# Optimization experiments

Hardware: AMD Instinct MI355X
Metric: run time of the kernel (lower is better)

## Reference

```python
import jax, jax.numpy as jnp
import numpy as np

B, D, U = 256, 2048, 2048  # batch, input_dim, units
EPS = 1e-8


def setup_inputs() -> dict:
    key = jax.random.key(0)
    ks = jax.random.split(key, 20)
    sd = 1.0 / np.sqrt(D)
    su = 1.0 / np.sqrt(U)
    inp = {
        'x': jax.random.normal(ks[0], (B, D), jnp.float32),
        'h_prev': jax.random.normal(ks[1], (B, U), jnp.float32),
        'c_prev': jax.random.normal(ks[2], (B, U), jnp.float32),
        'n_prev': jax.random.uniform(ks[3], (B, U), jnp.float32),
        'm_prev': jax.random.normal(ks[4], (B, U), jnp.float32),
        # input-to-gate weights (Dense with bias), keras layout [in, out]
        'Wz': jax.random.normal(ks[5], (D, U), jnp.float32) * sd,
        'Wi': jax.random.normal(ks[6], (D, U), jnp.float32) * sd,
        'Wf': jax.random.normal(ks[7], (D, U), jnp.float32) * sd,
        'Wo': jax.random.normal(ks[8], (D, U), jnp.float32) * sd,
        'bz': jnp.zeros((U,), jnp.float32),
        'bi': jnp.zeros((U,), jnp.float32),
        'bf': jnp.zeros((U,), jnp.float32),
        'bo': jnp.zeros((U,), jnp.float32),
        # recurrent weights (Dense without bias)
        'Uz': jax.random.normal(ks[9], (U, U), jnp.float32) * su,
        'Ui': jax.random.normal(ks[10], (U, U), jnp.float32) * su,
        'Uf': jax.random.normal(ks[11], (U, U), jnp.float32) * su,
        'Uo': jax.random.normal(ks[12], (U, U), jnp.float32) * su,
    }
    return inp


def reference(x, h_prev, c_prev, n_prev, m_prev,
              Wz, Wi, Wf, Wo, bz, bi, bf, bo, Uz, Ui, Uf, Uo):
    # fuse the 8 small GEMMs into 2 wide GEMMs (same math, gates split after)
    W = jnp.concatenate([Wz, Wi, Wf, Wo], axis=1)      # [D, 4U]
    Uc = jnp.concatenate([Uz, Ui, Uf, Uo], axis=1)     # [U, 4U]
    b = jnp.concatenate([bz, bi, bf, bo], axis=0)      # [4U]
    pre = x @ W + h_prev @ Uc + b                      # [B, 4U]
    z_tilde, i_tilde, f_tilde, o_tilde = jnp.split(pre, 4, axis=1)

    # exponential-gate stabilization (forget_gate_type='exponential')
    m_t = jnp.maximum(i_tilde + m_prev, i_tilde)
    i_t = jnp.exp(i_tilde - m_t)
    f_t = jnp.exp(f_tilde + m_prev - m_t)

    o_t = jax.nn.sigmoid(o_tilde)
    z_t = jnp.tanh(z_tilde)

    c_t = f_t * c_prev + i_t * z_t
    n_t = f_t * n_prev + i_t
    h_t = o_t * (c_t / (n_t + EPS))
    return jnp.stack([h_t, c_t, n_t, m_t], axis=0)  # [4, B, U]
```

## Files before the change

### kernel.cpp

```cpp
#include <hip/hip_runtime.h>
#include <cstdint>
#include <cstddef>

#define B_   256
#define D_   2048
#define U_   2048
#define NTOT 8192
#define BN   32
#define BK   64
#define KC   2048
#define ITERS (KC / BK)

typedef _Float16 half8 __attribute__((ext_vector_type(8)));
typedef float floatx16 __attribute__((ext_vector_type(16)));

__global__ __launch_bounds__(256) void prep_kernel(
    const float* __restrict__ x, const float* __restrict__ h,
    _Float16* __restrict__ Ahi)
{
    int gid   = blockIdx.x * 256 + threadIdx.x;
    int chunk = gid >> 8;
    int row   = gid & 255;
    int col0  = chunk * 8;
    const float* src = (col0 < D_) ? (x + row * D_ + col0)
                                   : (h + row * U_ + (col0 - D_));
    float4 v0 = *(const float4*)(src);
    float4 v1 = *(const float4*)(src + 4);
    float v[8] = {v0.x, v0.y, v0.z, v0.w, v1.x, v1.y, v1.z, v1.w};
    half8 hi;
#pragma unroll
    for (int i = 0; i < 8; ++i) hi[i] = (_Float16)v[i];
    *(half8*)(Ahi + (chunk * 256 + row) * 8) = hi;
}

__global__ __launch_bounds__(256, 2) void gemm_kernel(
    const _Float16* __restrict__ Ahi,
    const float* __restrict__ Wz, const float* __restrict__ Wi,
    const float* __restrict__ Wf, const float* __restrict__ Wo,
    const float* __restrict__ Uz, const float* __restrict__ Ui,
    const float* __restrict__ Uf, const float* __restrict__ Uo,
    float* __restrict__ P)
{
    __shared__ __align__(16) _Float16 sA[2][8 * 256 * 8];
    __shared__ __align__(16) _Float16 sB[2][BK * BN];

    const int t    = threadIdx.x;
    const int w    = t >> 6;
    const int lane = t & 63;
    const int lg   = lane >> 5;
    const int lm   = lane & 31;

    const int nblk = blockIdx.x;
    const int ks   = blockIdx.y;
    const int n0   = nblk * BN;
    const int g    = n0 >> 11;
    const int c0   = n0 & (U_ - 1);

    const float* wsel[8] = {Wz, Wi, Wf, Wo, Uz, Ui, Uf, Uo};
    const float* Bm = wsel[ks * 4 + g];
    const int chunk0 = ks * 256;

    const _Float16* Ag = Ahi + (size_t)chunk0 * 2048
                             + (size_t)(w * 8) * 512 + (size_t)lane * 8;

    const int scol = t & 31;
    const int sk0  = (t >> 5) * 8;
    const float* Bg = Bm + (size_t)sk0 * U_ + c0 + scol;
    const int swb = scol * 128 + ((sk0 * 2) ^ ((scol & 7) << 4));
    const int bswz = (lm & 7) << 4;

    const int aoff = lg * 4096 + (w * 64 + lm) * 16;

    floatx16 acc0 = {}, acc1 = {};
    float rbA[8], rbB[8];

#define ISSUE_A(tt, buf)                                                      \
    {                                                                         \
        _Pragma("unroll")                                                     \
        for (int i = 0; i < 8; ++i)                                           \
            __builtin_amdgcn_global_load_lds(                                 \
                (const __attribute__((address_space(1))) void*)(              \
                    Ag + (size_t)(tt) * 16384 + i * 512),                     \
                (__attribute__((address_space(3))) void*)(                    \
                    (char*)&sA[buf][0] + (w * 8 + i) * 1024 + lane * 16),     \
                16, 0, 0);                                                    \
    }

#define ISSUE_B(tt, rb)                                                       \
    {                                                                         \
        _Pragma("unroll")                                                     \
        for (int j = 0; j < 8; ++j)                                           \
            rb[j] = Bg[((size_t)(tt) * 64 + j) * U_];                         \
    }

#define WRITE_B(rb, buf)                                                      \
    {                                                                         \
        half8 hv;                                                             \
        _Pragma("unroll")                                                     \
        for (int j = 0; j < 8; ++j) hv[j] = (_Float16)rb[j];                  \
        *(half8*)((char*)&sB[buf][0] + swb) = hv;                             \
    }

#define COMPUTE(cur)                                                          \
    {                                                                         \
        const char* bA = (const char*)&sA[cur][0];                            \
        const char* bB = (const char*)&sB[cur][0];                            \
        half8 af0[4], af1[4], bfr[4];                                         \
        _Pragma("unroll")                                                     \
        for (int kin = 0; kin < 4; ++kin) {                                   \
            af0[kin] = *(const half8*)(bA + aoff + kin * 8192);               \
            af1[kin] = *(const half8*)(bA + aoff + kin * 8192 + 512);         \
            bfr[kin] = *(const half8*)(bB + lm * 128 +                        \
                ((kin * 32 + lg * 16) ^ bswz));                               \
        }                                                                     \
        __builtin_amdgcn_s_setprio(1);                                        \
        _Pragma("unroll")                                                     \
        for (int kin = 0; kin < 4; ++kin) {                                   \
            acc0 = __builtin_amdgcn_mfma_f32_32x32x16_f16(af0[kin], bfr[kin], acc0, 0, 0, 0); \
            acc1 = __builtin_amdgcn_mfma_f32_32x32x16_f16(af1[kin], bfr[kin], acc1, 0, 0, 0); \
        }                                                                     \
        __builtin_amdgcn_s_setprio(0);                                        \
    }

    ISSUE_B(0, rbA);
    ISSUE_A(0, 0);
    ISSUE_B(1, rbB);
    WRITE_B(rbA, 0);
    asm volatile("s_waitcnt vmcnt(8) lgkmcnt(0)" ::: "memory");
    __builtin_amdgcn_s_barrier();

    for (int tt = 0; tt < ITERS - 2; tt += 2) {
        ISSUE_A(tt + 1, 1);
        ISSUE_B(tt + 2, rbA);
        COMPUTE(0);
        WRITE_B(rbB, 1);
        asm volatile("s_waitcnt vmcnt(8) lgkmcnt(0)" ::: "memory");
        __builtin_amdgcn_s_barrier();

        ISSUE_A(tt + 2, 0);
        ISSUE_B(tt + 3, rbB);
        COMPUTE(1);
        WRITE_B(rbA, 0);
        asm volatile("s_waitcnt vmcnt(8) lgkmcnt(0)" ::: "memory");
        __builtin_amdgcn_s_barrier();
    }

    ISSUE_A(ITERS - 1, 1);
    COMPUTE(0);
    WRITE_B(rbB, 1);
    asm volatile("s_waitcnt vmcnt(0) lgkmcnt(0)" ::: "memory");
    __builtin_amdgcn_s_barrier();
    COMPUTE(1);

#undef ISSUE_A
#undef ISSUE_B
#undef WRITE_B
#undef COMPUTE

    float* Pks = P + (size_t)ks * ((size_t)B_ * NTOT);
#pragma unroll
    for (int r = 0; r < 16; ++r) {
        int m = w * 64 + 4 * lg + (r & 3) + 8 * (r >> 2);
        Pks[(size_t)m * NTOT + n0 + lm] = acc0[r];
    }
#pragma unroll
    for (int r = 0; r < 16; ++r) {
        int m = w * 64 + 32 + 4 * lg + (r & 3) + 8 * (r >> 2);
        Pks[(size_t)m * NTOT + n0 + lm] = acc1[r];
    }
}

__global__ __launch_bounds__(256) void gates_kernel(
    const float* __restrict__ P,
    const float* __restrict__ c_prev, const float* __restrict__ n_prev,
    const float* __restrict__ m_prev,
    const float* __restrict__ bz, const float* __restrict__ bi,
    const float* __restrict__ bf, const float* __restrict__ bo,
    float* __restrict__ out)
{
    const size_t PS = (size_t)B_ * NTOT;
    const int OS = B_ * U_;
    int gid = blockIdx.x * 256 + threadIdx.x;
    int m = gid >> 9;
    int u = (gid & 511) * 4;

    float pre[4][4];
#pragma unroll
    for (int gi = 0; gi < 4; ++gi) {
        const float* base = P + (size_t)m * NTOT + gi * U_ + u;
        float4 s0 = *(const float4*)(base);
        float4 s1 = *(const float4*)(base + PS);
        pre[gi][0] = s0.x + s1.x;
        pre[gi][1] = s0.y + s1.y;
        pre[gi][2] = s0.z + s1.z;
        pre[gi][3] = s0.w + s1.w;
    }
    float4 bzv = *(const float4*)(bz + u);
    float4 biv = *(const float4*)(bi + u);
    float4 bfv = *(const float4*)(bf + u);
    float4 bov = *(const float4*)(bo + u);
    float bza[4] = {bzv.x, bzv.y, bzv.z, bzv.w};
    float bia[4] = {biv.x, biv.y, biv.z, biv.w};
    float bfa[4] = {bfv.x, bfv.y, bfv.z, bfv.w};
    float boa[4] = {bov.x, bov.y, bov.z, bov.w};

    float4 cp4 = *(const float4*)(c_prev + m * U_ + u);
    float4 np4 = *(const float4*)(n_prev + m * U_ + u);
    float4 mp4 = *(const float4*)(m_prev + m * U_ + u);
    float cpa[4] = {cp4.x, cp4.y, cp4.z, cp4.w};
    float npa[4] = {np4.x, np4.y, np4.z, np4.w};
    float mpa[4] = {mp4.x, mp4.y, mp4.z, mp4.w};

    float hr[4], cr[4], nr[4], mr[4];
#pragma unroll
    for (int e = 0; e < 4; ++e) {
        float zt = pre[0][e] + bza[e];
        float it = pre[1][e] + bia[e];
        float ft = pre[2][e] + bfa[e];
        float ot = pre[3][e] + boa[e];
        float mp = mpa[e];
        float m_t = fmaxf(it + mp, it);
        float i_t = expf(it - m_t);
        float f_t = expf(ft + mp - m_t);
        float o_t = 1.0f / (1.0f + expf(-ot));
        float z_t = tanhf(zt);
        float c_t = f_t * cpa[e] + i_t * z_t;
        float n_t = f_t * npa[e] + i_t;
        float h_t = o_t * (c_t / (n_t + 1e-8f));
        hr[e] = h_t; cr[e] = c_t; nr[e] = n_t; mr[e] = m_t;
    }
    float4 hv = {hr[0], hr[1], hr[2], hr[3]};
    float4 cv = {cr[0], cr[1], cr[2], cr[3]};
    float4 nv = {nr[0], nr[1], nr[2], nr[3]};
    float4 mv = {mr[0], mr[1], mr[2], mr[3]};
    *(float4*)(out + 0 * OS + m * U_ + u) = hv;
    *(float4*)(out + 1 * OS + m * U_ + u) = cv;
    *(float4*)(out + 2 * OS + m * U_ + u) = nv;
    *(float4*)(out + 3 * OS + m * U_ + u) = mv;
}

extern "C" void kernel_launch(void* const* d_in, const int* in_sizes, int n_in,
                              void* d_out, int out_size, void* d_ws, size_t ws_size,
                              hipStream_t stream)
{
    const float* x  = (const float*)d_in[0];
    const float* h  = (const float*)d_in[1];
    const float* cp = (const float*)d_in[2];
    const float* np = (const float*)d_in[3];
    const float* mp = (const float*)d_in[4];
    const float* Wz = (const float*)d_in[5];
    const float* Wi = (const float*)d_in[6];
    const float* Wf = (const float*)d_in[7];
    const float* Wo = (const float*)d_in[8];
    const float* bz = (const float*)d_in[9];
    const float* bi = (const float*)d_in[10];
    const float* bf = (const float*)d_in[11];
    const float* bo = (const float*)d_in[12];
    const float* Uz = (const float*)d_in[13];
    const float* Ui = (const float*)d_in[14];
    const float* Uf = (const float*)d_in[15];
    const float* Uo = (const float*)d_in[16];

    float* P = (float*)d_ws;
    _Float16* Ahi = (_Float16*)((char*)d_ws + (size_t)2 * B_ * NTOT * sizeof(float));

    prep_kernel<<<512, 256, 0, stream>>>(x, h, Ahi);
    gemm_kernel<<<dim3(256, 2), 256, 0, stream>>>(Ahi,
        Wz, Wi, Wf, Wo, Uz, Ui, Uf, Uo, P);
    gates_kernel<<<512, 256, 0, stream>>>(P, cp, np, mp, bz, bi, bf, bo,
        (float*)d_out);
}
```

Measured before the change: 213.1 us.

## Give each wave its own A LDS slice and split vmcnt waits around compute

The A tile in shared memory is re-laid out so each wave loads and reads only its own contiguous slice, without the previous cross-wave interleave. The B-tile swizzle changes from an XOR pattern to a rotation. The single combined vmcnt/lgkmcnt wait before each barrier is split into separate vmcnt waits placed just before COMPUTE and WRITE_B, plus an lgkmcnt wait. The goal is to stop stalling on loads that the next step does not need yet, so global fetches overlap more with MFMA work. The new wait counts depend on exact issue order, and a miscount could read stale data; the new layout could also bring different LDS bank conflicts.

New measurement: 216.3 us. Within noise of the previous version (+1.5%).

```diff
diff --git a/kernel.cpp b/kernel.cpp
--- a/kernel.cpp
+++ b/kernel.cpp
@@ -41,7 +41,7 @@
     const float* __restrict__ Uf, const float* __restrict__ Uo,
     float* __restrict__ P)
 {
-    __shared__ __align__(16) _Float16 sA[2][8 * 256 * 8];
+    __shared__ __align__(16) _Float16 sA[2][4 * 8 * 64 * 8];
     __shared__ __align__(16) _Float16 sB[2][BK * BN];
 
     const int t    = threadIdx.x;
@@ -61,15 +61,12 @@
     const int chunk0 = ks * 256;
 
     const _Float16* Ag = Ahi + (size_t)chunk0 * 2048
-                             + (size_t)(w * 8) * 512 + (size_t)lane * 8;
+                             + (size_t)w * 512 + (size_t)lane * 8;
 
     const int scol = t & 31;
     const int sk0  = (t >> 5) * 8;
     const float* Bg = Bm + (size_t)sk0 * U_ + c0 + scol;
-    const int swb = scol * 128 + ((sk0 * 2) ^ ((scol & 7) << 4));
-    const int bswz = (lm & 7) << 4;
-
-    const int aoff = lg * 4096 + (w * 64 + lm) * 16;
+    const int swb = scol * 128 + ((sk0 * 2 + ((scol >> 2) << 4)) & 127);
 
     floatx16 acc0 = {}, acc1 = {};
     float rbA[8], rbB[8];
@@ -77,12 +74,12 @@
 #define ISSUE_A(tt, buf)                                                      \
     {                                                                         \
         _Pragma("unroll")                                                     \
-        for (int i = 0; i < 8; ++i)                                           \
+        for (int c = 0; c < 8; ++c)                                           \
             __builtin_amdgcn_global_load_lds(                                 \
                 (const __attribute__((address_space(1))) void*)(              \
-                    Ag + (size_t)(tt) * 16384 + i * 512),                     \
+                    Ag + (size_t)(tt) * 16384 + c * 2048),                    \
                 (__attribute__((address_space(3))) void*)(                    \
-                    (char*)&sA[buf][0] + (w * 8 + i) * 1024 + lane * 16),     \
+                    &sA[buf][w * 4096 + c * 512 + lane * 8]),                 \
                 16, 0, 0);                                                    \
     }
 
@@ -103,15 +100,15 @@
 
 #define COMPUTE(cur)                                                          \
     {                                                                         \
-        const char* bA = (const char*)&sA[cur][0];                            \
-        const char* bB = (const char*)&sB[cur][0];                            \
+        const _Float16* wA = &sA[cur][w * 4096];                              \
+        const char*     bB = (const char*)&sB[cur][0];                        \
         half8 af0[4], af1[4], bfr[4];                                         \
         _Pragma("unroll")                                                     \
         for (int kin = 0; kin < 4; ++kin) {                                   \
-            af0[kin] = *(const half8*)(bA + aoff + kin * 8192);               \
-            af1[kin] = *(const half8*)(bA + aoff + kin * 8192 + 512);         \
+            af0[kin] = *(const half8*)(wA + (kin * 2 + lg) * 512 + lm * 8);   \
+            af1[kin] = *(const half8*)(wA + (kin * 2 + lg) * 512 + lm * 8 + 256); \
             bfr[kin] = *(const half8*)(bB + lm * 128 +                        \
-                ((kin * 32 + lg * 16) ^ bswz));                               \
+                ((kin * 32 + lg * 16 + ((lm >> 2) << 4)) & 127));             \
         }                                                                     \
         __builtin_amdgcn_s_setprio(1);                                        \
         _Pragma("unroll")                                                     \
@@ -122,34 +119,42 @@
         __builtin_amdgcn_s_setprio(0);                                        \
     }
 
+    ISSUE_A(0, 0);
     ISSUE_B(0, rbA);
-    ISSUE_A(0, 0);
     ISSUE_B(1, rbB);
+    asm volatile("s_waitcnt vmcnt(8)" ::: "memory");
     WRITE_B(rbA, 0);
-    asm volatile("s_waitcnt vmcnt(8) lgkmcnt(0)" ::: "memory");
+    asm volatile("s_waitcnt lgkmcnt(0)" ::: "memory");
     __builtin_amdgcn_s_barrier();
 
     for (int tt = 0; tt < ITERS - 2; tt += 2) {
         ISSUE_A(tt + 1, 1);
         ISSUE_B(tt + 2, rbA);
+        asm volatile("s_waitcnt vmcnt(24)" ::: "memory");
         COMPUTE(0);
+        asm volatile("s_waitcnt vmcnt(16)" ::: "memory");
         WRITE_B(rbB, 1);
-        asm volatile("s_waitcnt vmcnt(8) lgkmcnt(0)" ::: "memory");
+        asm volatile("s_waitcnt lgkmcnt(0)" ::: "memory");
         __builtin_amdgcn_s_barrier();
 
         ISSUE_A(tt + 2, 0);
         ISSUE_B(tt + 3, rbB);
+        asm volatile("s_waitcnt vmcnt(24)" ::: "memory");
         COMPUTE(1);
+        asm volatile("s_waitcnt vmcnt(16)" ::: "memory");
         WRITE_B(rbA, 0);
-        asm volatile("s_waitcnt vmcnt(8) lgkmcnt(0)" ::: "memory");
+        asm volatile("s_waitcnt lgkmcnt(0)" ::: "memory");
         __builtin_amdgcn_s_barrier();
     }
 
     ISSUE_A(ITERS - 1, 1);
+    asm volatile("s_waitcnt vmcnt(16)" ::: "memory");
     COMPUTE(0);
+    asm volatile("s_waitcnt vmcnt(8)" ::: "memory");
     WRITE_B(rbB, 1);
-    asm volatile("s_waitcnt vmcnt(0) lgkmcnt(0)" ::: "memory");
+    asm volatile("s_waitcnt lgkmcnt(0)" ::: "memory");
     __builtin_amdgcn_s_barrier();
+    asm volatile("s_waitcnt vmcnt(0)" ::: "memory");
     COMPUTE(1);
 
 #undef ISSUE_A
```

## Retile GEMM to 128x128 blocks with 4-way split-K and fp16 partials

Applied to the files above, without the earlier changes.

Replaces the 256x32 full-batch tile (split-K 2) with 128x128 tiles over a 2x2 wave grid and split-K of 4. Each block now loads a quarter of the activation rows but four times as many weight columns, which cuts redundant A traffic through LDS. Partial sums are written as fp16 instead of fp32, halving workspace traffic, and the gates kernel sums four fp16 partials with 8 elements per thread. The cost is lower precision in the partial sums, more split-K reduction reads, and a block order that interleaves M tiles.

Result: faster. 206.2 us (-3.3%).

```diff
diff --git a/kernel.cpp b/kernel.cpp
--- a/kernel.cpp
+++ b/kernel.cpp
@@ -6,9 +6,11 @@
 #define D_   2048
 #define U_   2048
 #define NTOT 8192
-#define BN   32
+#define BM   128
+#define BN   128
 #define BK   64
-#define KC   2048
+#define KSP  4
+#define KC   1024
 #define ITERS (KC / BK)
 
 typedef _Float16 half8 __attribute__((ext_vector_type(8)));
@@ -33,91 +35,100 @@
     *(half8*)(Ahi + (chunk * 256 + row) * 8) = hi;
 }
 
-__global__ __launch_bounds__(256, 2) void gemm_kernel(
+__global__ __launch_bounds__(256) void gemm_kernel(
     const _Float16* __restrict__ Ahi,
     const float* __restrict__ Wz, const float* __restrict__ Wi,
     const float* __restrict__ Wf, const float* __restrict__ Wo,
     const float* __restrict__ Uz, const float* __restrict__ Ui,
     const float* __restrict__ Uf, const float* __restrict__ Uo,
-    float* __restrict__ P)
-{
-    __shared__ __align__(16) _Float16 sA[2][8 * 256 * 8];
-    __shared__ __align__(16) _Float16 sB[2][BK * BN];
+    _Float16* __restrict__ P)
+{
+    __shared__ __align__(16) _Float16 sA[2][8 * 128 * 8];
+    __shared__ __align__(16) _Float16 sB[2][8 * 128 * 8];
 
     const int t    = threadIdx.x;
     const int w    = t >> 6;
     const int lane = t & 63;
     const int lg   = lane >> 5;
     const int lm   = lane & 31;
-
-    const int nblk = blockIdx.x;
-    const int ks   = blockIdx.y;
-    const int n0   = nblk * BN;
-    const int g    = n0 >> 11;
-    const int c0   = n0 & (U_ - 1);
+    const int wm   = w >> 1;
+    const int wn   = w & 1;
+
+    const int bx = blockIdx.x;
+    const int mt = (bx >> 3) & 1;
+    const int nt = ((bx >> 4) << 3) | (bx & 7);
+    const int ks = blockIdx.y;
+
+    const int m0 = mt * BM;
+    const int n0 = nt * BN;
+    const int g  = n0 >> 11;
+    const int c0 = n0 & (U_ - 1);
 
     const float* wsel[8] = {Wz, Wi, Wf, Wo, Uz, Ui, Uf, Uo};
-    const float* Bm = wsel[ks * 4 + g];
-    const int chunk0 = ks * 256;
-
-    const _Float16* Ag = Ahi + (size_t)chunk0 * 2048
-                             + (size_t)(w * 8) * 512 + (size_t)lane * 8;
-
-    const int scol = t & 31;
-    const int sk0  = (t >> 5) * 8;
-    const float* Bg = Bm + (size_t)sk0 * U_ + c0 + scol;
-    const int swb = scol * 128 + ((sk0 * 2) ^ ((scol & 7) << 4));
-    const int bswz = (lm & 7) << 4;
-
-    const int aoff = lg * 4096 + (w * 64 + lm) * 16;
-
-    floatx16 acc0 = {}, acc1 = {};
-    float rbA[8], rbB[8];
+    const float* Bm = wsel[(ks >> 1) * 4 + g];
+    const int km = (ks & 1) * 1024;
+    const int chunkbase = ks * 128;
+
+    const int arow  = t & 127;
+    const int ahalf = t >> 7;
+
+    const int bcol  = t & 127;
+    const int sbase = (t >> 7) * 4;
+    const float* Bg = Bm + (size_t)km * U_ + c0 + bcol;
+
+    floatx16 acc00 = {}, acc01 = {}, acc10 = {}, acc11 = {};
+    float rbA[32], rbB[32];
 
 #define ISSUE_A(tt, buf)                                                      \
     {                                                                         \
         _Pragma("unroll")                                                     \
-        for (int i = 0; i < 8; ++i)                                           \
+        for (int i = 0; i < 4; ++i) {                                         \
+            int c = 2 * i + ahalf;                                            \
             __builtin_amdgcn_global_load_lds(                                 \
                 (const __attribute__((address_space(1))) void*)(              \
-                    Ag + (size_t)(tt) * 16384 + i * 512),                     \
+                    Ahi + (size_t)(chunkbase + (tt) * 8 + c) * 2048           \
+                        + (m0 + arow) * 8),                                   \
                 (__attribute__((address_space(3))) void*)(                    \
-                    (char*)&sA[buf][0] + (w * 8 + i) * 1024 + lane * 16),     \
+                    &sA[buf][i * 2048 + t * 8]),                              \
                 16, 0, 0);                                                    \
+        }                                                                     \
     }
 
 #define ISSUE_B(tt, rb)                                                       \
     {                                                                         \
         _Pragma("unroll")                                                     \
-        for (int j = 0; j < 8; ++j)                                           \
-            rb[j] = Bg[((size_t)(tt) * 64 + j) * U_];                         \
+        for (int sc = 0; sc < 4; ++sc)                                        \
+            _Pragma("unroll")                                                 \
+            for (int j = 0; j < 8; ++j)                                       \
+                rb[sc * 8 + j] =                                              \
+                    Bg[(size_t)((tt) * 64 + (sbase + sc) * 8 + j) * U_];      \
     }
 
 #define WRITE_B(rb, buf)                                                      \
     {                                                                         \
-        half8 hv;                                                             \
-        _Pragma("unroll")                                                     \
-        for (int j = 0; j < 8; ++j) hv[j] = (_Float16)rb[j];                  \
-        *(half8*)((char*)&sB[buf][0] + swb) = hv;                             \
+        _Pragma("unroll")                                                     \
+        for (int sc = 0; sc < 4; ++sc) {                                      \
+            half8 hv;                                                         \
+            _Pragma("unroll")                                                 \
+            for (int j = 0; j < 8; ++j) hv[j] = (_Float16)rb[sc * 8 + j];     \
+            *(half8*)(&sB[buf][(sbase + sc) * 1024 + bcol * 8]) = hv;         \
+        }                                                                     \
     }
 
 #define COMPUTE(cur)                                                          \
     {                                                                         \
-        const char* bA = (const char*)&sA[cur][0];                            \
-        const char* bB = (const char*)&sB[cur][0];                            \
-        half8 af0[4], af1[4], bfr[4];                                         \
+        __builtin_amdgcn_s_setprio(1);                                        \
         _Pragma("unroll")                                                     \
         for (int kin = 0; kin < 4; ++kin) {                                   \
-            af0[kin] = *(const half8*)(bA + aoff + kin * 8192);               \
-            af1[kin] = *(const half8*)(bA + aoff + kin * 8192 + 512);         \
-            bfr[kin] = *(const half8*)(bB + lm * 128 +                        \
-                ((kin * 32 + lg * 16) ^ bswz));                               \
-        }                                                                     \
-        __builtin_amdgcn_s_setprio(1);                                        \
-        _Pragma("unroll")                                                     \
-        for (int kin = 0; kin < 4; ++kin) {                                   \
-            acc0 = __builtin_amdgcn_mfma_f32_32x32x16_f16(af0[kin], bfr[kin], acc0, 0, 0, 0); \
-            acc1 = __builtin_amdgcn_mfma_f32_32x32x16_f16(af1[kin], bfr[kin], acc1, 0, 0, 0); \
+            int cs = kin * 2 + lg;                                            \
+            half8 a0 = *(const half8*)(&sA[cur][cs * 1024 + (wm * 64 + lm) * 8]);       \
+            half8 a1 = *(const half8*)(&sA[cur][cs * 1024 + (wm * 64 + 32 + lm) * 8]);  \
+            half8 b0 = *(const half8*)(&sB[cur][cs * 1024 + (wn * 64 + lm) * 8]);       \
+            half8 b1 = *(const half8*)(&sB[cur][cs * 1024 + (wn * 64 + 32 + lm) * 8]);  \
+            acc00 = __builtin_amdgcn_mfma_f32_32x32x16_f16(a0, b0, acc00, 0, 0, 0);     \
+            acc01 = __builtin_amdgcn_mfma_f32_32x32x16_f16(a0, b1, acc01, 0, 0, 0);     \
+            acc10 = __builtin_amdgcn_mfma_f32_32x32x16_f16(a1, b0, acc10, 0, 0, 0);     \
+            acc11 = __builtin_amdgcn_mfma_f32_32x32x16_f16(a1, b1, acc11, 0, 0, 0);     \
         }                                                                     \
         __builtin_amdgcn_s_setprio(0);                                        \
     }
@@ -125,28 +136,32 @@
     ISSUE_B(0, rbA);
     ISSUE_A(0, 0);
     ISSUE_B(1, rbB);
+    asm volatile("s_waitcnt vmcnt(36)" ::: "memory");
     WRITE_B(rbA, 0);
-    asm volatile("s_waitcnt vmcnt(8) lgkmcnt(0)" ::: "memory");
+    asm volatile("s_waitcnt vmcnt(32) lgkmcnt(0)" ::: "memory");
     __builtin_amdgcn_s_barrier();
 
     for (int tt = 0; tt < ITERS - 2; tt += 2) {
         ISSUE_A(tt + 1, 1);
         ISSUE_B(tt + 2, rbA);
         COMPUTE(0);
+        asm volatile("s_waitcnt vmcnt(36)" ::: "memory");
         WRITE_B(rbB, 1);
-        asm volatile("s_waitcnt vmcnt(8) lgkmcnt(0)" ::: "memory");
+        asm volatile("s_waitcnt vmcnt(32) lgkmcnt(0)" ::: "memory");
         __builtin_amdgcn_s_barrier();
 
         ISSUE_A(tt + 2, 0);
         ISSUE_B(tt + 3, rbB);
         COMPUTE(1);
+        asm volatile("s_waitcnt vmcnt(36)" ::: "memory");
         WRITE_B(rbA, 0);
-        asm volatile("s_waitcnt vmcnt(8) lgkmcnt(0)" ::: "memory");
+        asm volatile("s_waitcnt vmcnt(32) lgkmcnt(0)" ::: "memory");
         __builtin_amdgcn_s_barrier();
     }
 
     ISSUE_A(ITERS - 1, 1);
     COMPUTE(0);
+    asm volatile("s_waitcnt vmcnt(4)" ::: "memory");
     WRITE_B(rbB, 1);
     asm volatile("s_waitcnt vmcnt(0) lgkmcnt(0)" ::: "memory");
     __builtin_amdgcn_s_barrier();
@@ -157,21 +172,24 @@
 #undef WRITE_B
 #undef COMPUTE
 
-    float* Pks = P + (size_t)ks * ((size_t)B_ * NTOT);
-#pragma unroll
-    for (int r = 0; r < 16; ++r) {
-        int m = w * 64 + 4 * lg + (r & 3) + 8 * (r >> 2);
-        Pks[(size_t)m * NTOT + n0 + lm] = acc0[r];
-    }
-#pragma unroll
-    for (int r = 0; r < 16; ++r) {
-        int m = w * 64 + 32 + 4 * lg + (r & 3) + 8 * (r >> 2);
-        Pks[(size_t)m * NTOT + n0 + lm] = acc1[r];
-    }
+    _Float16* Pks = P + (size_t)ks * ((size_t)B_ * NTOT);
+    const floatx16* accs[4] = {&acc00, &acc01, &acc10, &acc11};
+#pragma unroll
+    for (int mi = 0; mi < 2; ++mi)
+#pragma unroll
+        for (int ni = 0; ni < 2; ++ni) {
+            const floatx16& a = *accs[mi * 2 + ni];
+            int colg = n0 + wn * 64 + ni * 32 + lm;
+#pragma unroll
+            for (int r = 0; r < 16; ++r) {
+                int m = m0 + wm * 64 + mi * 32 + 4 * lg + (r & 3) + 8 * (r >> 2);
+                Pks[(size_t)m * NTOT + colg] = (_Float16)a[r];
+            }
+        }
 }
 
 __global__ __launch_bounds__(256) void gates_kernel(
-    const float* __restrict__ P,
+    const _Float16* __restrict__ P,
     const float* __restrict__ c_prev, const float* __restrict__ n_prev,
     const float* __restrict__ m_prev,
     const float* __restrict__ bz, const float* __restrict__ bi,
@@ -181,39 +199,42 @@
     const size_t PS = (size_t)B_ * NTOT;
     const int OS = B_ * U_;
     int gid = blockIdx.x * 256 + threadIdx.x;
-    int m = gid >> 9;
-    int u = (gid & 511) * 4;
-
-    float pre[4][4];
+    int m = gid >> 8;
+    int u = (gid & 255) * 8;
+
+    float pre[4][8];
 #pragma unroll
     for (int gi = 0; gi < 4; ++gi) {
-        const float* base = P + (size_t)m * NTOT + gi * U_ + u;
-        float4 s0 = *(const float4*)(base);
-        float4 s1 = *(const float4*)(base + PS);
-        pre[gi][0] = s0.x + s1.x;
-        pre[gi][1] = s0.y + s1.y;
-        pre[gi][2] = s0.z + s1.z;
-        pre[gi][3] = s0.w + s1.w;
-    }
-    float4 bzv = *(const float4*)(bz + u);
-    float4 biv = *(const float4*)(bi + u);
-    float4 bfv = *(const float4*)(bf + u);
-    float4 bov = *(const float4*)(bo + u);
-    float bza[4] = {bzv.x, bzv.y, bzv.z, bzv.w};
-    float bia[4] = {biv.x, biv.y, biv.z, biv.w};
-    float bfa[4] = {bfv.x, bfv.y, bfv.z, bfv.w};
-    float boa[4] = {bov.x, bov.y, bov.z, bov.w};
-
-    float4 cp4 = *(const float4*)(c_prev + m * U_ + u);
-    float4 np4 = *(const float4*)(n_prev + m * U_ + u);
-    float4 mp4 = *(const float4*)(m_prev + m * U_ + u);
-    float cpa[4] = {cp4.x, cp4.y, cp4.z, cp4.w};
-    float npa[4] = {np4.x, np4.y, np4.z, np4.w};
-    float mpa[4] = {mp4.x, mp4.y, mp4.z, mp4.w};
-
-    float hr[4], cr[4], nr[4], mr[4];
-#pragma unroll
-    for (int e = 0; e < 4; ++e) {
+#pragma unroll
+        for (int e = 0; e < 8; ++e) pre[gi][e] = 0.0f;
+#pragma unroll
+        for (int ksp = 0; ksp < 4; ++ksp) {
+            half8 v = *(const half8*)(P + (size_t)ksp * PS
+                                        + (size_t)m * NTOT + gi * 2048 + u);
+#pragma unroll
+            for (int e = 0; e < 8; ++e) pre[gi][e] += (float)v[e];
+        }
+    }
+
+    float bza[8], bia[8], bfa[8], boa[8], cpa[8], npa[8], mpa[8];
+    *(float4*)(bza)     = *(const float4*)(bz + u);
+    *(float4*)(bza + 4) = *(const float4*)(bz + u + 4);
+    *(float4*)(bia)     = *(const float4*)(bi + u);
+    *(float4*)(bia + 4) = *(const float4*)(bi + u + 4);
+    *(float4*)(bfa)     = *(const float4*)(bf + u);
+    *(float4*)(bfa + 4) = *(const float4*)(bf + u + 4);
+    *(float4*)(boa)     = *(const float4*)(bo + u);
+    *(float4*)(boa + 4) = *(const float4*)(bo + u + 4);
+    *(float4*)(cpa)     = *(const float4*)(c_prev + m * U_ + u);
+    *(float4*)(cpa + 4) = *(const float4*)(c_prev + m * U_ + u + 4);
+    *(float4*)(npa)     = *(const float4*)(n_prev + m * U_ + u);
+    *(float4*)(npa + 4) = *(const float4*)(n_prev + m * U_ + u + 4);
+    *(float4*)(mpa)     = *(const float4*)(m_prev + m * U_ + u);
+    *(float4*)(mpa + 4) = *(const float4*)(m_prev + m * U_ + u + 4);
+
+    float hr[8], cr[8], nr[8], mr[8];
+#pragma unroll
+    for (int e = 0; e < 8; ++e) {
         float zt = pre[0][e] + bza[e];
         float it = pre[1][e] + bia[e];
         float ft = pre[2][e] + bfa[e];
@@ -229,14 +250,15 @@
         float h_t = o_t * (c_t / (n_t + 1e-8f));
         hr[e] = h_t; cr[e] = c_t; nr[e] = n_t; mr[e] = m_t;
     }
-    float4 hv = {hr[0], hr[1], hr[2], hr[3]};
-    float4 cv = {cr[0], cr[1], cr[2], cr[3]};
-    float4 nv = {nr[0], nr[1], nr[2], nr[3]};
-    float4 mv = {mr[0], mr[1], mr[2], mr[3]};
-    *(float4*)(out + 0 * OS + m * U_ + u) = hv;
-    *(float4*)(out + 1 * OS + m * U_ + u) = cv;
-    *(float4*)(out + 2 * OS + m * U_ + u) = nv;
-    *(float4*)(out + 3 * OS + m * U_ + u) = mv;
+    float* ob = out + m * U_ + u;
+    *(float4*)(ob + 0 * OS)     = *(float4*)(hr);
+    *(float4*)(ob + 0 * OS + 4) = *(float4*)(hr + 4);
+    *(float4*)(ob + 1 * OS)     = *(float4*)(cr);
+    *(float4*)(ob + 1 * OS + 4) = *(float4*)(cr + 4);
+    *(float4*)(ob + 2 * OS)     = *(float4*)(nr);
+    *(float4*)(ob + 2 * OS + 4) = *(float4*)(nr + 4);
+    *(float4*)(ob + 3 * OS)     = *(float4*)(mr);
+    *(float4*)(ob + 3 * OS + 4) = *(float4*)(mr + 4);
 }
 
 extern "C" void kernel_launch(void* const* d_in, const int* in_sizes, int n_in,
@@ -261,12 +283,13 @@
     const float* Uf = (const float*)d_in[15];
     const float* Uo = (const float*)d_in[16];
 
-    float* P = (float*)d_ws;
-    _Float16* Ahi = (_Float16*)((char*)d_ws + (size_t)2 * B_ * NTOT * sizeof(float));
+    _Float16* P   = (_Float16*)d_ws;
+    _Float16* Ahi = (_Float16*)((char*)d_ws
+                     + (size_t)KSP * B_ * NTOT * sizeof(_Float16));
 
     prep_kernel<<<512, 256, 0, stream>>>(x, h, Ahi);
-    gemm_kernel<<<dim3(256, 2), 256, 0, stream>>>(Ahi,
+    gemm_kernel<<<dim3(128, KSP), 256, 0, stream>>>(Ahi,
         Wz, Wi, Wf, Wo, Uz, Ui, Uf, Uo, P);
-    gates_kernel<<<512, 256, 0, stream>>>(P, cp, np, mp, bz, bi, bf, bo,
+    gates_kernel<<<256, 256, 0, stream>>>(P, cp, np, mp, bz, bi, bf, bo,
         (float*)d_out);
 }
```
